# Kernel tuning notes

Hardware: AMD Instinct MI355X
Metric: run time of the kernel (lower is better)

## Reference

```python
import jax, jax.numpy as jnp
import numpy as np

DIM = 1024
N_HEADS = 16
HEAD_DIM = DIM // N_HEADS
B, T = 2, 2048


def setup_inputs() -> dict:
    key = jax.random.key(0)
    ks = jax.random.split(key, 5)
    x = jax.random.normal(ks[0], (B, T, DIM), dtype=jnp.float32)
    s = DIM ** -0.5
    Wq = jax.random.normal(ks[1], (DIM, DIM), dtype=jnp.float32) * s
    Wk = jax.random.normal(ks[2], (DIM, DIM), dtype=jnp.float32) * s
    Wv = jax.random.normal(ks[3], (DIM, DIM), dtype=jnp.float32) * s
    Wo = jax.random.normal(ks[4], (DIM, DIM), dtype=jnp.float32) * s
    # causal mask: 1 where attendable, 0 where masked (masked_fill on mask==0)
    mask = jnp.tril(jnp.ones((T, T), dtype=jnp.int32))[None, None, :, :]
    return {"x": x, "Wq": Wq, "Wk": Wk, "Wv": Wv, "Wo": Wo, "mask": mask}


def _rope_tables(seq_len, dim, dtype):
    inv_freq = 1.0 / (10000.0 ** (jnp.arange(0, dim, 2, dtype=jnp.float32) / dim))
    t = jnp.arange(seq_len, dtype=jnp.float32)
    freqs = jnp.outer(t, inv_freq)               # [T, dim/2]
    emb = jnp.concatenate([freqs, freqs], -1)    # [T, dim]
    return jnp.cos(emb).astype(dtype), jnp.sin(emb).astype(dtype)


def _rotate_half(t):
    h = t.shape[-1] // 2
    return jnp.concatenate([-t[..., h:], t[..., :h]], axis=-1)


def reference(x, Wq, Wk, Wv, Wo, mask):
    Bq, Tq, C = x.shape
    H, Dh = N_HEADS, C // N_HEADS
    q = (x @ Wq.T).reshape(Bq, Tq, H, Dh)
    k = (x @ Wk.T).reshape(Bq, Tq, H, Dh)
    v = (x @ Wv.T).reshape(Bq, Tq, H, Dh)
    cos, sin = _rope_tables(Tq, Dh, x.dtype)
    cos = cos[None, :, None, :]   # [1,T,1,Dh]
    sin = sin[None, :, None, :]
    q = q * cos + _rotate_half(q) * sin
    k = k * cos + _rotate_half(k) * sin
    scale = Dh ** -0.5
    # [B,H,T,T]
    attn = jnp.einsum('bqhd,bkhd->bhqk', q, k) * scale
    attn = jnp.where(mask == 0, jnp.float32(-jnp.inf).astype(attn.dtype), attn)
    attn = jax.nn.softmax(attn, axis=-1)
    out = jnp.einsum('bhqk,bkhd->bqhd', attn, v).reshape(Bq, Tq, C)
    return out @ Wo.T
```

## Files before the change

kernel.cpp:

```cpp
#include <hip/hip_runtime.h>
#include <stdint.h>


typedef float  f32x4  __attribute__((ext_vector_type(4)));
typedef __bf16 bf16x8 __attribute__((ext_vector_type(8)));

#define GLDS16(gp, lp)                                                         \
  __builtin_amdgcn_global_load_lds(                                            \
      (const __attribute__((address_space(1))) void*)(gp),                     \
      (__attribute__((address_space(3))) void*)(lp), 16, 0, 0)

static __device__ __forceinline__ f32x4 zero4() {
  f32x4 z = {0.f, 0.f, 0.f, 0.f};
  return z;
}

static __device__ __forceinline__ bf16x8 cvt8(const float* __restrict__ p) {
  f32x4 u = *(const f32x4*)p;
  f32x4 v = *(const f32x4*)(p + 4);
  bf16x8 o;
#pragma unroll
  for (int j = 0; j < 4; ++j) o[j] = (__bf16)u[j];
#pragma unroll
  for (int j = 0; j < 4; ++j) o[4 + j] = (__bf16)v[j];
  return o;
}

template <int N>
static __device__ __forceinline__ float ror16(float x) {
  int v = __builtin_amdgcn_update_dpp(0, __float_as_int(x),
                                      0x120 | N, 0xF, 0xF, true);
  return __int_as_float(v);
}

static __device__ __forceinline__ float redmax16(float x) {
  x = fmaxf(x, ror16<1>(x));
  x = fmaxf(x, ror16<2>(x));
  x = fmaxf(x, ror16<4>(x));
  x = fmaxf(x, ror16<8>(x));
  return x;
}

static __device__ __forceinline__ float redsum16(float x) {
  x += ror16<1>(x);
  x += ror16<2>(x);
  x += ror16<4>(x);
  x += ror16<8>(x);
  return x;
}

__global__ __launch_bounds__(256) void prep(
    const float* __restrict__ x,
    const float* __restrict__ Wq, const float* __restrict__ Wk,
    const float* __restrict__ Wv, const float* __restrict__ Wo,
    __bf16* __restrict__ xb, __bf16* __restrict__ Wb)
{
  size_t g = ((size_t)blockIdx.x * 256 + threadIdx.x) * 8;
  if (g < (size_t)4194304) {
    *(bf16x8*)&xb[g] = cvt8(x + g);
  } else {
    size_t j = g - 4194304;
    int w = (int)(j >> 20);
    size_t off = j & 1048575;
    const float* src = (w == 0) ? Wq : (w == 1) ? Wk : (w == 2) ? Wv : Wo;
    *(bf16x8*)&Wb[(size_t)w * 1048576 + off] = cvt8(src + off);
  }
}

__global__ __launch_bounds__(256) void gemm_qkv(
    const __bf16* __restrict__ xb, const __bf16* __restrict__ Wb,
    __bf16* __restrict__ Qp, __bf16* __restrict__ Kp, __bf16* __restrict__ Vt)
{
  __shared__ __bf16 As[128 * 32];
  __shared__ __bf16 Bs[128 * 32];
  __shared__ __bf16 Es[4 * 16 * 72];

  const int tid  = threadIdx.x;
  const int lane = tid & 63;
  const int wid  = tid >> 6;
  const int quad = lane >> 4;
  const int l16  = lane & 15;
  const int wm   = (wid >> 1) * 64;
  const int wn   = (wid & 1) * 64;

  const int lin = blockIdx.x;
  const int n0  = (lin & 7) * 128;
  const int r2  = lin >> 3;
  const int z   = r2 % 3;
  const int m0  = (r2 / 3) * 128;
  const __bf16* Bt = Wb + (size_t)z * 1048576;

  const int r0 = tid >> 2, c0 = tid & 3;
  const int r1 = (tid + 256) >> 2;

  f32x4 acc[4][4];
  for (int i = 0; i < 4; ++i)
    for (int j = 0; j < 4; ++j) acc[i][j] = zero4();

  for (int k0 = 0; k0 < 1024; k0 += 32) {
    __syncthreads();
    GLDS16(xb + (size_t)(m0 + r0) * 1024 + k0 + c0 * 8, &As[(size_t)tid * 8]);
    GLDS16(xb + (size_t)(m0 + r1) * 1024 + k0 + c0 * 8, &As[(size_t)(tid + 256) * 8]);
    GLDS16(Bt + (size_t)(n0 + r0) * 1024 + k0 + c0 * 8, &Bs[(size_t)tid * 8]);
    GLDS16(Bt + (size_t)(n0 + r1) * 1024 + k0 + c0 * 8, &Bs[(size_t)(tid + 256) * 8]);
    __syncthreads();

    bf16x8 af[4], bfr[4];
    for (int i = 0; i < 4; ++i)
      af[i] = *(const bf16x8*)&As[(wm + i * 16 + l16) * 32 + quad * 8];
    for (int i = 0; i < 4; ++i)
      bfr[i] = *(const bf16x8*)&Bs[(wn + i * 16 + l16) * 32 + quad * 8];
    for (int mt = 0; mt < 4; ++mt)
      for (int nt = 0; nt < 4; ++nt)
        acc[mt][nt] = __builtin_amdgcn_mfma_f32_16x16x32_bf16(
            af[mt], bfr[nt], acc[mt][nt], 0, 0, 0);
  }

  const int h = (n0 + wn) >> 6;
  __bf16* es = &Es[wid * 1152];
  const int rl = lane >> 3, ch = lane & 7;

  if (z < 2) {
    const float c0f = -13.287712379549449f / 32.0f;
    const float f0 = exp2f((float)l16 * c0f);
    const float f1 = exp2f((float)(16 + l16) * c0f);
    const float SC = (z == 0) ? 0.125f * 1.44269504088896340736f : 1.0f;
    for (int mt = 0; mt < 4; ++mt)
      for (int r = 0; r < 4; ++r) {
        int gm = m0 + wm + mt * 16 + 4 * quad + r;
        float t = (float)(gm & 2047);
        for (int nt = 0; nt < 2; ++nt) {
          float ang = t * (nt ? f1 : f0);
          float cv = __cosf(ang) * SC, sv = __sinf(ang) * SC;
          float lo = acc[mt][nt][r], hi = acc[mt][nt + 2][r];
          acc[mt][nt][r]     = lo * cv - hi * sv;
          acc[mt][nt + 2][r] = hi * cv + lo * sv;
        }
      }
    __bf16* dst = (z == 0) ? Qp : Kp;
    for (int mt = 0; mt < 4; ++mt) {
      for (int nt = 0; nt < 4; ++nt)
        for (int r = 0; r < 4; ++r)
          es[(4 * quad + r) * 72 + nt * 16 + l16] = (__bf16)acc[mt][nt][r];
      size_t g0 = (size_t)(m0 + wm + mt * 16 + rl) * 1024 + n0 + wn + ch * 8;
      *(bf16x8*)&dst[g0]            = *(const bf16x8*)&es[rl * 72 + ch * 8];
      *(bf16x8*)&dst[g0 + 8 * 1024] = *(const bf16x8*)&es[(rl + 8) * 72 + ch * 8];
    }
  } else {
    const int b = m0 >> 11;
    const size_t hb = (size_t)(b * 16 + h) * 64;
    const int tt = (m0 + wm) & 2047;
    for (int nt = 0; nt < 4; ++nt) {
      for (int mt = 0; mt < 4; ++mt)
        for (int r = 0; r < 4; ++r)
          es[l16 * 72 + mt * 16 + 4 * quad + r] = (__bf16)acc[mt][nt][r];
      size_t g0 = (hb + nt * 16 + rl) * 2048 + tt + ch * 8;
      *(bf16x8*)&Vt[g0]                     = *(const bf16x8*)&es[rl * 72 + ch * 8];
      *(bf16x8*)&Vt[g0 + (size_t)8 * 2048]  = *(const bf16x8*)&es[(rl + 8) * 72 + ch * 8];
    }
  }
}

__global__ __launch_bounds__(256) void attn_fwd(
    __bf16* QA, const __bf16* __restrict__ Kp,
    const __bf16* __restrict__ Vt)
{
  __shared__ __bf16 Ks[64 * 72];
  __shared__ __bf16 Vs[64 * 72];
  __shared__ __bf16 Ps[64 * 72];

  const int tid  = threadIdx.x;
  const int lane = tid & 63, wid = tid >> 6;
  const int quad = lane >> 4, l16 = lane & 15;

  const int L  = blockIdx.x;
  const int Lp = (L & 7) * 64 + (L >> 3);
  const int bh = Lp >> 4;
  const int xq = Lp & 15;
  const int b = bh >> 4, h = bh & 15;

  const size_t rowb = (size_t)b * 2048;
  const __bf16* Vb = Vt + (size_t)bh * 64 * 2048;

  const int sr0 = tid >> 3, sc0 = tid & 7;
  const int sr1 = (tid + 256) >> 3;

  for (int pass = 0; pass < 2; ++pass) {
    const int qb = pass ? (31 - xq) : xq;
    const int q0 = qb * 64;

    bf16x8 qa[2];
    for (int ks = 0; ks < 2; ++ks)
      qa[ks] = *(const bf16x8*)
          &QA[(rowb + q0 + wid * 16 + l16) * 1024 + h * 64 + ks * 32 + quad * 8];

    f32x4 oacc[4];
    for (int i = 0; i < 4; ++i) oacc[i] = zero4();
    float m_i[4], l_i[4];
    for (int r = 0; r < 4; ++r) { m_i[r] = -1e30f; l_i[r] = 0.f; }

    const int kcmax = qb;

    bf16x8 k0v = *(const bf16x8*)&Kp[(rowb + sr0) * 1024 + h * 64 + sc0 * 8];
    bf16x8 k1v = *(const bf16x8*)&Kp[(rowb + sr1) * 1024 + h * 64 + sc0 * 8];
    bf16x8 v0v = *(const bf16x8*)&Vb[(size_t)sr0 * 2048 + sc0 * 8];
    bf16x8 v1v = *(const bf16x8*)&Vb[(size_t)sr1 * 2048 + sc0 * 8];

    for (int kc = 0; kc <= kcmax; ++kc) {
      __syncthreads();
      *(bf16x8*)&Ks[sr0 * 72 + sc0 * 8] = k0v;
      *(bf16x8*)&Ks[sr1 * 72 + sc0 * 8] = k1v;
      *(bf16x8*)&Vs[sr0 * 72 + sc0 * 8] = v0v;
      *(bf16x8*)&Vs[sr1 * 72 + sc0 * 8] = v1v;
      __syncthreads();

      if (kc < kcmax) {
        const int kn = kc + 1;
        k0v = *(const bf16x8*)&Kp[(rowb + kn * 64 + sr0) * 1024 + h * 64 + sc0 * 8];
        k1v = *(const bf16x8*)&Kp[(rowb + kn * 64 + sr1) * 1024 + h * 64 + sc0 * 8];
        v0v = *(const bf16x8*)&Vb[(size_t)sr0 * 2048 + kn * 64 + sc0 * 8];
        v1v = *(const bf16x8*)&Vb[(size_t)sr1 * 2048 + kn * 64 + sc0 * 8];
      }

      f32x4 sacc[4];
      for (int i = 0; i < 4; ++i) sacc[i] = zero4();
      __builtin_amdgcn_s_setprio(1);
      for (int ks = 0; ks < 2; ++ks) {
        bf16x8 qf = qa[ks];
        for (int nt = 0; nt < 4; ++nt) {
          bf16x8 kf = *(const bf16x8*)
              &Ks[(nt * 16 + l16) * 72 + ks * 32 + quad * 8];
          sacc[nt] = __builtin_amdgcn_mfma_f32_16x16x32_bf16(
              qf, kf, sacc[nt], 0, 0, 0);
        }
      }
      __builtin_amdgcn_s_setprio(0);

      const bool diag = (kc == kcmax);
      float rmax[4] = {-1e30f, -1e30f, -1e30f, -1e30f};
      for (int nt = 0; nt < 4; ++nt)
        for (int r = 0; r < 4; ++r) {
          float s = sacc[nt][r];
          if (diag) {
            int i = wid * 16 + 4 * quad + r;
            int j = nt * 16 + l16;
            if (j > i) s = -1e30f;
          }
          sacc[nt][r] = s;
          rmax[r] = fmaxf(rmax[r], s);
        }
      for (int r = 0; r < 4; ++r)
        rmax[r] = redmax16(rmax[r]);

      float alpha[4], rsum[4];
      for (int r = 0; r < 4; ++r) {
        float nm = fmaxf(m_i[r], rmax[r]);
        alpha[r] = __builtin_amdgcn_exp2f(m_i[r] - nm);
        m_i[r] = nm;
        rsum[r] = 0.f;
      }
      for (int nt = 0; nt < 4; ++nt)
        for (int r = 0; r < 4; ++r) {
          float p = __builtin_amdgcn_exp2f(sacc[nt][r] - m_i[r]);
          rsum[r] += p;
          Ps[(wid * 16 + 4 * quad + r) * 72 + nt * 16 + l16] = (__bf16)p;
        }
      for (int r = 0; r < 4; ++r) {
        rsum[r] = redsum16(rsum[r]);
        l_i[r] = l_i[r] * alpha[r] + rsum[r];
        for (int nt = 0; nt < 4; ++nt) oacc[nt][r] *= alpha[r];
      }

      __builtin_amdgcn_s_setprio(1);
      for (int ks = 0; ks < 2; ++ks) {
        bf16x8 pf = *(const bf16x8*)
            &Ps[(wid * 16 + l16) * 72 + ks * 32 + quad * 8];
        for (int nt = 0; nt < 4; ++nt) {
          bf16x8 vf = *(const bf16x8*)
              &Vs[(nt * 16 + l16) * 72 + ks * 32 + quad * 8];
          oacc[nt] = __builtin_amdgcn_mfma_f32_16x16x32_bf16(
              pf, vf, oacc[nt], 0, 0, 0);
        }
      }
      __builtin_amdgcn_s_setprio(0);
    }

    for (int r = 0; r < 4; ++r) {
      float inv = 1.f / l_i[r];
      for (int nt = 0; nt < 4; ++nt)
        Ps[(wid * 16 + 4 * quad + r) * 72 + nt * 16 + l16] =
            (__bf16)(oacc[nt][r] * inv);
    }
    __syncthreads();
    {
      int row = tid >> 3, ch = tid & 7;
      size_t g0 = (rowb + q0 + row) * 1024 + h * 64 + ch * 8;
      *(bf16x8*)&QA[g0]                   = *(const bf16x8*)&Ps[row * 72 + ch * 8];
      *(bf16x8*)&QA[g0 + (size_t)32 * 1024] =
          *(const bf16x8*)&Ps[(row + 32) * 72 + ch * 8];
    }
    __syncthreads();
  }
}

__global__ __launch_bounds__(256) void gemm_out(
    const __bf16* __restrict__ AO, const __bf16* __restrict__ Wob,
    float* __restrict__ Of)
{
  __shared__ __bf16 As[128 * 32];
  __shared__ __bf16 Bs[128 * 32];
  __shared__ float  EsF[4 * 16 * 68];

  const int tid  = threadIdx.x;
  const int lane = tid & 63;
  const int wid  = tid >> 6;
  const int quad = lane >> 4;
  const int l16  = lane & 15;
  const int wm   = (wid >> 1) * 64;
  const int wn   = (wid & 1) * 64;
  const int lin = blockIdx.x;
  const int n0  = (lin & 7) * 128;
  const int m0  = (lin >> 3) * 128;

  const int r0 = tid >> 2, c0 = tid & 3;
  const int r1 = (tid + 256) >> 2;

  f32x4 acc[4][4];
  for (int i = 0; i < 4; ++i)
    for (int j = 0; j < 4; ++j) acc[i][j] = zero4();

  for (int k0 = 0; k0 < 1024; k0 += 32) {
    __syncthreads();
    GLDS16(AO  + (size_t)(m0 + r0) * 1024 + k0 + c0 * 8, &As[(size_t)tid * 8]);
    GLDS16(AO  + (size_t)(m0 + r1) * 1024 + k0 + c0 * 8, &As[(size_t)(tid + 256) * 8]);
    GLDS16(Wob + (size_t)(n0 + r0) * 1024 + k0 + c0 * 8, &Bs[(size_t)tid * 8]);
    GLDS16(Wob + (size_t)(n0 + r1) * 1024 + k0 + c0 * 8, &Bs[(size_t)(tid + 256) * 8]);
    __syncthreads();

    bf16x8 af[4], bfr[4];
    for (int i = 0; i < 4; ++i)
      af[i] = *(const bf16x8*)&As[(wm + i * 16 + l16) * 32 + quad * 8];
    for (int i = 0; i < 4; ++i)
      bfr[i] = *(const bf16x8*)&Bs[(wn + i * 16 + l16) * 32 + quad * 8];
    for (int mt = 0; mt < 4; ++mt)
      for (int nt = 0; nt < 4; ++nt)
        acc[mt][nt] = __builtin_amdgcn_mfma_f32_16x16x32_bf16(
            af[mt], bfr[nt], acc[mt][nt], 0, 0, 0);
  }

  float* es = &EsF[wid * 1088];
  const int rl = lane >> 4, ch = lane & 15;
  for (int mt = 0; mt < 4; ++mt) {
    for (int nt = 0; nt < 4; ++nt)
      for (int r = 0; r < 4; ++r)
        es[(4 * quad + r) * 68 + nt * 16 + l16] = acc[mt][nt][r];
    size_t g0 = (size_t)(m0 + wm + mt * 16 + rl) * 1024 + n0 + wn + ch * 4;
    *(f32x4*)&Of[g0]             = *(const f32x4*)&es[rl * 68 + ch * 4];
    *(f32x4*)&Of[g0 + 4 * 1024]  = *(const f32x4*)&es[(rl + 4) * 68 + ch * 4];
    *(f32x4*)&Of[g0 + 8 * 1024]  = *(const f32x4*)&es[(rl + 8) * 68 + ch * 4];
    *(f32x4*)&Of[g0 + 12 * 1024] = *(const f32x4*)&es[(rl + 12) * 68 + ch * 4];
  }
}

__global__ __launch_bounds__(256) void copy_bf16x8(
    const __bf16* __restrict__ src, __bf16* __restrict__ dst)
{
  size_t i = ((size_t)blockIdx.x * 256 + threadIdx.x) * 8;
  *(bf16x8*)&dst[i] = *(const bf16x8*)&src[i];
}

extern "C" void kernel_launch(void* const* d_in, const int* in_sizes, int n_in,
                              void* d_out, int out_size, void* d_ws, size_t ws_size,
                              hipStream_t stream) {
  const float* x  = (const float*)d_in[0];
  const float* Wq = (const float*)d_in[1];
  const float* Wk = (const float*)d_in[2];
  const float* Wv = (const float*)d_in[3];
  const float* Wo = (const float*)d_in[4];
  float* out = (float*)d_out;

  const size_t NELT = (size_t)4194304;
  __bf16* Qp = (__bf16*)d_ws;
  __bf16* Kp = Qp + NELT;
  __bf16* Vt = Kp + NELT;
  __bf16* xb = (__bf16*)d_out;
  __bf16* Wb = xb + NELT;

  prep<<<dim3(4096), 256, 0, stream>>>(x, Wq, Wk, Wv, Wo, xb, Wb);
  gemm_qkv<<<dim3(768), 256, 0, stream>>>(xb, Wb, Qp, Kp, Vt);
  attn_fwd<<<dim3(512), 256, 0, stream>>>(Qp, Kp, Vt);
  copy_bf16x8<<<dim3(512), 256, 0, stream>>>(Wb + 3 * NELT / 4, Kp);
  gemm_out<<<dim3(256), 256, 0, stream>>>(Qp, Kp, out);
}
```

Before: 212.2 us.

## Transpose QK^T MFMA so each lane owns one query row; add lazy rescaling

The QK^T MFMA operands are swapped so that S^T is computed, which makes each lane hold all scores for a single query row. Row max and row sum now need one scalar each, combined with two cross-lane xor shuffles instead of four DPP reductions per row. Rescaling of the accumulator is skipped whenever no lane's max grows past the running max by more than 8 (log2 domain), which saves exp and multiply work. The trade-off is extra shuffles to broadcast alpha and 1/l into the PV accumulator layout, and a bounded growth of P values up to 2^8 before rounding to bf16.

Result: faster. 200.3 us (-5.6%).

```diff
diff --git a/kernel.cpp b/kernel.cpp
--- a/kernel.cpp
+++ b/kernel.cpp
@@ -4,6 +4,7 @@
 
 typedef float  f32x4  __attribute__((ext_vector_type(4)));
 typedef __bf16 bf16x8 __attribute__((ext_vector_type(8)));
+typedef __bf16 bf16x4 __attribute__((ext_vector_type(4)));
 
 #define GLDS16(gp, lp)                                                         \
   __builtin_amdgcn_global_load_lds(                                            \
@@ -24,29 +25,6 @@
 #pragma unroll
   for (int j = 0; j < 4; ++j) o[4 + j] = (__bf16)v[j];
   return o;
-}
-
-template <int N>
-static __device__ __forceinline__ float ror16(float x) {
-  int v = __builtin_amdgcn_update_dpp(0, __float_as_int(x),
-                                      0x120 | N, 0xF, 0xF, true);
-  return __int_as_float(v);
-}
-
-static __device__ __forceinline__ float redmax16(float x) {
-  x = fmaxf(x, ror16<1>(x));
-  x = fmaxf(x, ror16<2>(x));
-  x = fmaxf(x, ror16<4>(x));
-  x = fmaxf(x, ror16<8>(x));
-  return x;
-}
-
-static __device__ __forceinline__ float redsum16(float x) {
-  x += ror16<1>(x);
-  x += ror16<2>(x);
-  x += ror16<4>(x);
-  x += ror16<8>(x);
-  return x;
 }
 
 __global__ __launch_bounds__(256) void prep(
@@ -196,8 +174,7 @@
 
     f32x4 oacc[4];
     for (int i = 0; i < 4; ++i) oacc[i] = zero4();
-    float m_i[4], l_i[4];
-    for (int r = 0; r < 4; ++r) { m_i[r] = -1e30f; l_i[r] = 0.f; }
+    float m_i = -1e30f, l_i = 0.f;
 
     const int kcmax = qb;
 
@@ -227,48 +204,57 @@
       __builtin_amdgcn_s_setprio(1);
       for (int ks = 0; ks < 2; ++ks) {
         bf16x8 qf = qa[ks];
-        for (int nt = 0; nt < 4; ++nt) {
+        for (int mt = 0; mt < 4; ++mt) {
           bf16x8 kf = *(const bf16x8*)
-              &Ks[(nt * 16 + l16) * 72 + ks * 32 + quad * 8];
-          sacc[nt] = __builtin_amdgcn_mfma_f32_16x16x32_bf16(
-              qf, kf, sacc[nt], 0, 0, 0);
+              &Ks[(mt * 16 + l16) * 72 + ks * 32 + quad * 8];
+          sacc[mt] = __builtin_amdgcn_mfma_f32_16x16x32_bf16(
+              kf, qf, sacc[mt], 0, 0, 0);
         }
       }
       __builtin_amdgcn_s_setprio(0);
 
       const bool diag = (kc == kcmax);
-      float rmax[4] = {-1e30f, -1e30f, -1e30f, -1e30f};
-      for (int nt = 0; nt < 4; ++nt)
+      float rmax = -1e30f;
+      const int iq = wid * 16 + l16;
+      for (int mt = 0; mt < 4; ++mt)
         for (int r = 0; r < 4; ++r) {
-          float s = sacc[nt][r];
-          if (diag) {
-            int i = wid * 16 + 4 * quad + r;
-            int j = nt * 16 + l16;
-            if (j > i) s = -1e30f;
-          }
-          sacc[nt][r] = s;
-          rmax[r] = fmaxf(rmax[r], s);
-        }
-      for (int r = 0; r < 4; ++r)
-        rmax[r] = redmax16(rmax[r]);
-
-      float alpha[4], rsum[4];
-      for (int r = 0; r < 4; ++r) {
-        float nm = fmaxf(m_i[r], rmax[r]);
-        alpha[r] = __builtin_amdgcn_exp2f(m_i[r] - nm);
-        m_i[r] = nm;
-        rsum[r] = 0.f;
-      }
-      for (int nt = 0; nt < 4; ++nt)
+          float s = sacc[mt][r];
+          if (diag && (mt * 16 + 4 * quad + r > iq)) s = -1e30f;
+          sacc[mt][r] = s;
+          rmax = fmaxf(rmax, s);
+        }
+      rmax = fmaxf(rmax, __shfl_xor(rmax, 16, 64));
+      rmax = fmaxf(rmax, __shfl_xor(rmax, 32, 64));
+
+      const bool noresc = __all(rmax <= m_i + 8.0f);
+      float alpha = 1.0f;
+      if (!noresc) {
+        float nm = fmaxf(m_i, rmax);
+        alpha = __builtin_amdgcn_exp2f(m_i - nm);
+        m_i = nm;
+      }
+
+      float rsum = 0.f;
+      for (int mt = 0; mt < 4; ++mt) {
+        bf16x4 pw;
         for (int r = 0; r < 4; ++r) {
-          float p = __builtin_amdgcn_exp2f(sacc[nt][r] - m_i[r]);
-          rsum[r] += p;
-          Ps[(wid * 16 + 4 * quad + r) * 72 + nt * 16 + l16] = (__bf16)p;
-        }
-      for (int r = 0; r < 4; ++r) {
-        rsum[r] = redsum16(rsum[r]);
-        l_i[r] = l_i[r] * alpha[r] + rsum[r];
-        for (int nt = 0; nt < 4; ++nt) oacc[nt][r] *= alpha[r];
+          float p = __builtin_amdgcn_exp2f(sacc[mt][r] - m_i);
+          rsum += p;
+          pw[r] = (__bf16)p;
+        }
+        *(bf16x4*)&Ps[iq * 72 + mt * 16 + 4 * quad] = pw;
+      }
+      rsum += __shfl_xor(rsum, 16, 64);
+      rsum += __shfl_xor(rsum, 32, 64);
+
+      if (!noresc) {
+        l_i = l_i * alpha + rsum;
+        for (int r = 0; r < 4; ++r) {
+          float a_r = __shfl(alpha, 4 * quad + r, 64);
+          for (int nt = 0; nt < 4; ++nt) oacc[nt][r] *= a_r;
+        }
+      } else {
+        l_i += rsum;
       }
 
       __builtin_amdgcn_s_setprio(1);
@@ -285,11 +271,14 @@
       __builtin_amdgcn_s_setprio(0);
     }
 
-    for (int r = 0; r < 4; ++r) {
-      float inv = 1.f / l_i[r];
-      for (int nt = 0; nt < 4; ++nt)
-        Ps[(wid * 16 + 4 * quad + r) * 72 + nt * 16 + l16] =
-            (__bf16)(oacc[nt][r] * inv);
+    {
+      float invl = 1.0f / l_i;
+      for (int r = 0; r < 4; ++r) {
+        float inv_r = __shfl(invl, 4 * quad + r, 64);
+        for (int nt = 0; nt < 4; ++nt)
+          Ps[(wid * 16 + 4 * quad + r) * 72 + nt * 16 + l16] =
+              (__bf16)(oacc[nt][r] * inv_r);
+      }
     }
     __syncthreads();
     {
```
